# Kernel tuning notes

Hardware: AMD Instinct MI355X
Metric: run time of the kernel (lower is better)

Reference implementation:

```python
import jax, jax.numpy as jnp
import numpy as np

R = 4  # num_relations


def rgcn_conv(x, src, dst, etype, W, root, bias):
    """PyG RGCNConv (aggr='mean', no self-loops):
    out_i = x_i @ root + bias + sum_r mean_{j in N_r(i)} (x_j @ W_r)
    x: [N,D], W: [R,D,H], root: [D,H], bias: [H]
    """
    N = x.shape[0]
    Rr, _, H = W.shape
    x_r = jnp.einsum('nd,rdh->rnh', x, W)          # [R,N,H] relation-transformed feats
    msg = x_r[etype, src]                          # [E,H] per-edge messages
    seg = etype * N + dst                          # combined (relation, dst) segment id
    sums = jax.ops.segment_sum(msg, seg, num_segments=Rr * N)            # [R*N,H]
    cnt = jax.ops.segment_sum(jnp.ones(msg.shape[0], msg.dtype), seg,
                              num_segments=Rr * N)                        # [R*N]
    mean = sums / jnp.maximum(cnt, 1.0)[:, None]
    agg = mean.reshape(Rr, N, H).sum(0)            # sum over relations
    return agg + x @ root + bias


def setup_inputs() -> dict:
    key = jax.random.key(0)
    ks = jax.random.split(key, 12)
    N, E, D, H, ED = 20000, 320000, 256, 256, 64
    s = lambda fan: 1.0 / np.sqrt(fan)
    return {
        'x': jax.random.normal(ks[0], (N, D), jnp.float32),
        'edge_index': jax.random.randint(ks[1], (2, E), 0, N),
        'edge_type': jax.random.randint(ks[2], (E,), 0, R),
        'edge_attr': jax.random.normal(ks[3], (E, ED), jnp.float32),
        'W0': jax.random.normal(ks[4], (R, D, H), jnp.float32) * s(D),
        'root0': jax.random.normal(ks[5], (D, H), jnp.float32) * s(D),
        'b0': jnp.zeros((H,), jnp.float32),
        'W1': jax.random.normal(ks[6], (R, H, H), jnp.float32) * s(H),
        'root1': jax.random.normal(ks[7], (H, H), jnp.float32) * s(H),
        'b1': jnp.zeros((H,), jnp.float32),
        'lin_w': jax.random.normal(ks[8], (H, 2), jnp.float32) * s(H),
        'lin_b': jnp.zeros((2,), jnp.float32),
    }


def reference(x, edge_index, edge_type, edge_attr, W0, root0, b0, W1, root1, b1, lin_w, lin_b):
    src, dst = edge_index[0], edge_index[1]
    h = jax.nn.relu(rgcn_conv(x, src, dst, edge_type, W0, root0, b0))
    h = rgcn_conv(h, src, dst, edge_type, W1, root1, b1)
    g = h.sum(axis=0, keepdims=True)   # global_add_pool, single graph -> [1,H]
    # dropout inactive in eval mode
    return g @ lin_w + lin_b           # [1,2]
```

## Files before the change

### kernel.cpp

```cpp
#include <hip/hip_runtime.h>
#include <hip/hip_bf16.h>

#define RREL 4
#define DIM 256
#define KDIM 1280
#define KMEAN 1024
#define BCAP 32
#define WROWS 64

__device__ __forceinline__ float bf2f(unsigned short u) {
    union { unsigned int i; float f; } z; z.i = ((unsigned int)u) << 16; return z.f;
}
__device__ __forceinline__ unsigned short f2bf(float f) {
    __hip_bfloat16 h = __float2bfloat16(f);
    return *(unsigned short*)&h;
}

typedef __attribute__((ext_vector_type(8))) short bf16x8;
typedef __attribute__((ext_vector_type(8))) unsigned short u16x8;
typedef __attribute__((ext_vector_type(4))) float f32x4;
typedef __attribute__((ext_vector_type(4))) float fx4;


__global__ __launch_bounds__(256)
void prep(const int* __restrict__ etype, const int* __restrict__ src,
          const int* __restrict__ dst,
          int* __restrict__ counts, int* __restrict__ bucket, int N, int E,
          const float* __restrict__ x, __hip_bfloat16* __restrict__ xb, int n4,
          const float* __restrict__ W0, const float* __restrict__ root0,
          __hip_bfloat16* __restrict__ WT,
          int eb, int cb) {
    int b = blockIdx.x;
    if (b < eb) {
        int e = b * 256 + threadIdx.x;
        if (e < E) {
            int seg = etype[e] * N + dst[e];
            int p = atomicAdd(&counts[seg], 1);
            if (p < BCAP) bucket[(size_t)seg * BCAP + p] = src[e];
        }
    } else if (b < eb + cb) {
        int i = (b - eb) * 256 + threadIdx.x;
        if (i < n4) {
            fx4 v = *((const fx4*)x + i);
            ushort4 u = make_ushort4(f2bf(v.x), f2bf(v.y), f2bf(v.z), f2bf(v.w));
            ((ushort4*)xb)[i] = u;
        }
    } else {
        __shared__ float tile[32][33];
        int q = b - eb - cb;
        int nblk = q / 40;
        int kblk = q - nblk * 40;
        int k0 = kblk * 32, n0 = nblk * 32;
        int tx = threadIdx.x & 31, ty = threadIdx.x >> 5;
        const float* srcp;
        int kbase;
        if (k0 < RREL * DIM) { srcp = W0; kbase = k0; } else { srcp = root0; kbase = k0 - RREL * DIM; }
#pragma unroll
        for (int j = 0; j < 4; j++) {
            int k = kbase + ty + j * 8;
            tile[ty + j * 8][tx] = srcp[(size_t)k * DIM + n0 + tx];
        }
        __syncthreads();
#pragma unroll
        for (int j = 0; j < 4; j++) {
            int n = n0 + ty + j * 8;
            WT[(size_t)n * KDIM + k0 + tx] = __float2bfloat16(tile[tx][ty + j * 8]);
        }
    }
}


__global__ __launch_bounds__(256)
void aggregate(const __hip_bfloat16* __restrict__ feat, const int* __restrict__ counts,
               const int* __restrict__ bucket, __hip_bfloat16* __restrict__ Y, int N,
               const int* __restrict__ etype, const int* __restrict__ srcv,
               const int* __restrict__ dstv, float* __restrict__ wsr, int E, int ab) {
    if ((int)blockIdx.x >= ab) {
        int e = (blockIdx.x - ab) * 256 + threadIdx.x;
        if (e < E) {
            int r = etype[e];
            int seg = r * N + dstv[e];
            float sc = 1.f / (float)counts[seg];
            atomicAdd(&wsr[(size_t)srcv[e] * RREL + r], sc);
        }
        return;
    }
    int r = threadIdx.x >> 6, lane = threadIdx.x & 63;
    int h = lane >> 5, li = lane & 31;
    int i = blockIdx.x * 2 + h;
    if (i >= N) return;
    int seg = r * N + i;
    int cnt = min(counts[seg], BCAP);
    const unsigned short* fu = (const unsigned short*)feat;
    const int* bk = bucket + (size_t)seg * BCAP;
    float a[8] = {};
    for (int k = 0; k < cnt; k += 4) {
        int4 q = *(const int4*)(bk + k);
        float m1 = (k + 1 < cnt) ? 1.f : 0.f;
        float m2 = (k + 2 < cnt) ? 1.f : 0.f;
        float m3 = (k + 3 < cnt) ? 1.f : 0.f;
        int i0 = q.x;
        int i1 = m1 ? q.y : q.x;
        int i2 = m2 ? q.z : q.x;
        int i3 = m3 ? q.w : q.x;
        u16x8 v0 = *(const u16x8*)(fu + (size_t)i0 * DIM + li * 8);
        u16x8 v1 = *(const u16x8*)(fu + (size_t)i1 * DIM + li * 8);
        u16x8 v2 = *(const u16x8*)(fu + (size_t)i2 * DIM + li * 8);
        u16x8 v3 = *(const u16x8*)(fu + (size_t)i3 * DIM + li * 8);
#pragma unroll
        for (int j = 0; j < 8; j++)
            a[j] += bf2f(v0[j]) + m1 * bf2f(v1[j]) + m2 * bf2f(v2[j]) + m3 * bf2f(v3[j]);
    }
    float inv = (cnt > 0) ? 1.f / (float)cnt : 0.f;
    u16x8 u;
#pragma unroll
    for (int j = 0; j < 8; j++) u[j] = f2bf(a[j] * inv);
    __builtin_nontemporal_store(u,
        (u16x8*)((unsigned short*)Y + (size_t)i * KMEAN + r * DIM + li * 8));
}


#define BMg 64
#define BKg 64

__global__ __launch_bounds__(256)
void gemm_mfma(const __hip_bfloat16* __restrict__ A,
               const __hip_bfloat16* __restrict__ Aself,
               const __hip_bfloat16* __restrict__ Bt,
               const float* __restrict__ bias,
               unsigned short* __restrict__ Cbf,
               int Nrows) {
    __shared__ short As[2][BMg * BKg];
    __shared__ short Bs[2][DIM * BKg];
    int t = threadIdx.x;
    int lane = t & 63;
    int w = t >> 6;
    size_t row0 = (size_t)blockIdx.x * BMg;

    const unsigned short* Ag = (const unsigned short*)A;
    const unsigned short* Sg = (const unsigned short*)Aself;
    const unsigned short* Bg = (const unsigned short*)Bt;

    float bb[4];
#pragma unroll
    for (int ni = 0; ni < 4; ni++) bb[ni] = bias[w * 64 + ni * 16 + (lane & 15)];

    f32x4 acc[4][4] = {};

    auto issue_tile = [&](int k0, short* as, short* bs) {
        const unsigned short* Abase;
        int kk, stride;
        if (k0 < KMEAN) { Abase = Ag; kk = k0; stride = KMEAN; }
        else            { Abase = Sg; kk = k0 - KMEAN; stride = DIM; }
#pragma unroll
        for (int h = 0; h < 2; h++) {
            int c = t + h * 256;
            int r = c >> 3, pl = c & 7, pg = pl ^ (r & 7);
            const unsigned short* ga = Abase + (row0 + r) * stride + kk + pg * 8;
            __builtin_amdgcn_global_load_lds(
                (const __attribute__((address_space(1))) void*)ga,
                (__attribute__((address_space(3))) void*)((char*)as + c * 16),
                16, 0, 0);
        }
#pragma unroll
        for (int h = 0; h < 8; h++) {
            int c = t + h * 256;
            int r = c >> 3, pl = c & 7, pg = pl ^ (r & 7);
            const unsigned short* gb = Bg + (size_t)r * KDIM + k0 + pg * 8;
            __builtin_amdgcn_global_load_lds(
                (const __attribute__((address_space(1))) void*)gb,
                (__attribute__((address_space(3))) void*)((char*)bs + c * 16),
                16, 0, 0);
        }
    };

    issue_tile(0, As[0], Bs[0]);
    int cur = 0;
    for (int k0 = 0; k0 < KDIM; k0 += BKg) {
        __syncthreads();
        if (k0 + BKg < KDIM) issue_tile(k0 + BKg, As[cur ^ 1], Bs[cur ^ 1]);
        const short* as = As[cur];
        const short* bs = Bs[cur];
#pragma unroll
        for (int ks = 0; ks < 2; ks++) {
            int p = ks * 4 + (lane >> 4);
            bf16x8 af[4], bfr[4];
#pragma unroll
            for (int mi = 0; mi < 4; mi++) {
                int m = mi * 16 + (lane & 15);
                af[mi] = *(const bf16x8*)&as[m * 64 + (p ^ (m & 7)) * 8];
            }
#pragma unroll
            for (int ni = 0; ni < 4; ni++) {
                int n = w * 64 + ni * 16 + (lane & 15);
                bfr[ni] = *(const bf16x8*)&bs[n * 64 + (p ^ (n & 7)) * 8];
            }
#pragma unroll
            for (int mi = 0; mi < 4; mi++)
#pragma unroll
                for (int ni = 0; ni < 4; ni++)
                    acc[mi][ni] = __builtin_amdgcn_mfma_f32_16x16x32_bf16(af[mi], bfr[ni], acc[mi][ni], 0, 0, 0);
        }
        cur ^= 1;
    }

#pragma unroll
    for (int mi = 0; mi < 4; mi++) {
#pragma unroll
        for (int j = 0; j < 4; j++) {
            size_t row = row0 + mi * 16 + (lane >> 4) * 4 + j;
            if (row < (size_t)Nrows) {
#pragma unroll
                for (int ni = 0; ni < 4; ni++) {
                    size_t col = w * 64 + ni * 16 + (lane & 15);
                    float v = fmaxf(acc[mi][ni][j] + bb[ni], 0.f);
                    Cbf[row * DIM + col] = f2bf(v);
                }
            }
        }
    }
}


__global__ __launch_bounds__(256)
void wcolsum(const unsigned short* __restrict__ h1, const float* __restrict__ wsr,
             int N, float* __restrict__ sv) {
    int t = threadIdx.x;
    int i0 = blockIdx.x * WROWS;
    int iend = min(i0 + WROWS, N);
    float a0 = 0.f, a1 = 0.f, a2 = 0.f, a3 = 0.f, as = 0.f;
#pragma unroll 4
    for (int i = i0; i < iend; i++) {
        float v = bf2f(h1[(size_t)i * DIM + t]);
        fx4 wv = *(const fx4*)(wsr + (size_t)i * RREL);
        as += v;
        a0 += wv.x * v; a1 += wv.y * v; a2 += wv.z * v; a3 += wv.w * v;
    }
    atomicAdd(&sv[0 * DIM + t], a0);
    atomicAdd(&sv[1 * DIM + t], a1);
    atomicAdd(&sv[2 * DIM + t], a2);
    atomicAdd(&sv[3 * DIM + t], a3);
    atomicAdd(&sv[4 * DIM + t], as);
}


__global__ __launch_bounds__(256)
void gemv(const float* __restrict__ sv, const float* __restrict__ W1,
          const float* __restrict__ root1, const float* __restrict__ b1,
          int N, float* __restrict__ g) {
    int t = threadIdx.x;
    int kk0 = blockIdx.x * 32;
    float acc = 0.f;
    for (int kk = kk0; kk < kk0 + 32; kk++) {
        int r = kk >> 8;
        int k = kk & 255;
        const float* row = (r < RREL) ? (W1 + ((size_t)r * DIM + k) * DIM)
                                      : (root1 + (size_t)k * DIM);
        acc += sv[kk] * row[t];
    }
    if (blockIdx.x == 0) acc += (float)N * b1[t];
    atomicAdd(&g[t], acc);
}


__global__ void final_lin(const float* __restrict__ g, const float* __restrict__ lw,
                          const float* __restrict__ lb, float* __restrict__ out) {
    __shared__ float s0[256], s1[256];
    int t = threadIdx.x;
    float gv = g[t];
    s0[t] = gv * lw[t * 2 + 0];
    s1[t] = gv * lw[t * 2 + 1];
    __syncthreads();
    for (int off = 128; off > 0; off >>= 1) {
        if (t < off) { s0[t] += s0[t + off]; s1[t] += s1[t + off]; }
        __syncthreads();
    }
    if (t == 0) { out[0] = s0[0] + lb[0]; out[1] = s1[0] + lb[1]; }
}


static inline char* align_up(char* p, size_t a) {
    return (char*)(((uintptr_t)p + (a - 1)) & ~(uintptr_t)(a - 1));
}

extern "C" void kernel_launch(void* const* d_in, const int* in_sizes, int n_in,
                              void* d_out, int out_size, void* d_ws, size_t ws_size,
                              hipStream_t stream) {
    const float* x     = (const float*)d_in[0];
    const int*   eidx  = (const int*)d_in[1];
    const int*   etype = (const int*)d_in[2];
    const float* W0    = (const float*)d_in[4];
    const float* root0 = (const float*)d_in[5];
    const float* b0    = (const float*)d_in[6];
    const float* W1    = (const float*)d_in[7];
    const float* root1 = (const float*)d_in[8];
    const float* b1    = (const float*)d_in[9];
    const float* lin_w = (const float*)d_in[10];
    const float* lin_b = (const float*)d_in[11];
    float* out = (float*)d_out;

    const int N = in_sizes[0] / DIM;
    const int E = in_sizes[2];
    const int RN = RREL * N;
    const int* src = eidx;
    const int* dst = eidx + E;

    const int gx = (N + BMg - 1) / BMg;
    const int Mpad = gx * BMg;

    char* w = (char*)d_ws;
    int*   counts = (int*)w;   w += (size_t)RN * 4;
    float* wsr    = (float*)w; w += (size_t)N * RREL * 4;
    float* sv     = (float*)w; w += (size_t)5 * DIM * 4;
    float* g      = (float*)w; w += 256 * 4;
    size_t zero_bytes = (size_t)RN * 4 + (size_t)N * RREL * 4 + 5 * DIM * 4 + 256 * 4;
    int* bucket = (int*)w; w += (size_t)RN * BCAP * 4;
    w = align_up(w, 16);
    __hip_bfloat16* WT = (__hip_bfloat16*)w; w += (size_t)DIM * KDIM * 2;
    w = align_up(w, 16);
    __hip_bfloat16* Y  = (__hip_bfloat16*)w; w += (size_t)Mpad * KMEAN * 2;
    __hip_bfloat16* xb = (__hip_bfloat16*)w; w += (size_t)Mpad * DIM * 2;
    __hip_bfloat16* h1 = (__hip_bfloat16*)w; w += (size_t)Mpad * DIM * 2;

    hipMemsetAsync(counts, 0, zero_bytes, stream);

    int eb = (E + 255) / 256;
    int n4 = N * DIM / 4;
    int cb = (n4 + 255) / 256;
    int wb = (KDIM / 32) * (DIM / 32);

    prep<<<eb + cb + wb, 256, 0, stream>>>(etype, src, dst, counts, bucket, N, E,
                                           x, xb, n4, W0, root0, WT, eb, cb);

    int ab = (N + 1) / 2;
    aggregate<<<ab + eb, 256, 0, stream>>>(xb, counts, bucket, Y, N,
                                           etype, src, dst, wsr, E, ab);
    gemm_mfma<<<gx, 256, 0, stream>>>(Y, xb, WT, b0, (unsigned short*)h1, N);
    wcolsum<<<(N + WROWS - 1) / WROWS, 256, 0, stream>>>((const unsigned short*)h1, wsr, N, sv);
    gemv<<<KDIM / 32, 256, 0, stream>>>(sv, W1, root1, b1, N, g);

    final_lin<<<1, 256, 0, stream>>>(g, lin_w, lin_b, out);
}
```

Measured before the change: 256.7 us.

## Fuse weighted column-sum into GEMM epilogue and merge gemv with final linear

The GEMM epilogue now computes per-column sums of the ReLU output, plus sums weighted by the relation weights, directly from the accumulators. It reduces them across lanes with shuffles and atomically adds them into sv. This removes the h1 buffer write/read and the separate wcolsum launch. The gemv kernel also absorbs final_lin through a last-block-done counter, saving a launch, at the cost of extra atomics and a fence.

```diff
diff --git a/kernel.cpp b/kernel.cpp
--- a/kernel.cpp
+++ b/kernel.cpp
@@ -6,7 +6,6 @@
 #define KDIM 1280
 #define KMEAN 1024
 #define BCAP 32
-#define WROWS 64
 
 __device__ __forceinline__ float bf2f(unsigned short u) {
     union { unsigned int i; float f; } z; z.i = ((unsigned int)u) << 16; return z.f;
@@ -128,7 +127,8 @@
                const __hip_bfloat16* __restrict__ Aself,
                const __hip_bfloat16* __restrict__ Bt,
                const float* __restrict__ bias,
-               unsigned short* __restrict__ Cbf,
+               const float* __restrict__ wsr,
+               float* __restrict__ sv,
                int Nrows) {
     __shared__ short As[2][BMg * BKg];
     __shared__ short Bs[2][DIM * BKg];
@@ -204,50 +204,51 @@
         cur ^= 1;
     }
 
+    float a[4][5];
+#pragma unroll
+    for (int ni = 0; ni < 4; ni++)
+#pragma unroll
+        for (int s = 0; s < 5; s++) a[ni][s] = 0.f;
+
 #pragma unroll
     for (int mi = 0; mi < 4; mi++) {
 #pragma unroll
         for (int j = 0; j < 4; j++) {
             size_t row = row0 + mi * 16 + (lane >> 4) * 4 + j;
             if (row < (size_t)Nrows) {
+                fx4 wv = *(const fx4*)(wsr + row * RREL);
 #pragma unroll
                 for (int ni = 0; ni < 4; ni++) {
-                    size_t col = w * 64 + ni * 16 + (lane & 15);
                     float v = fmaxf(acc[mi][ni][j] + bb[ni], 0.f);
-                    Cbf[row * DIM + col] = f2bf(v);
+                    a[ni][4] += v;
+                    a[ni][0] += wv.x * v;
+                    a[ni][1] += wv.y * v;
+                    a[ni][2] += wv.z * v;
+                    a[ni][3] += wv.w * v;
                 }
             }
         }
     }
+#pragma unroll
+    for (int ni = 0; ni < 4; ni++) {
+        int col = w * 64 + ni * 16 + (lane & 15);
+#pragma unroll
+        for (int s = 0; s < 5; s++) {
+            float v = a[ni][s];
+            v += __shfl_xor(v, 16, 64);
+            v += __shfl_xor(v, 32, 64);
+            if ((lane >> 4) == 0) atomicAdd(&sv[s * DIM + col], v);
+        }
+    }
 }
 
 
 __global__ __launch_bounds__(256)
-void wcolsum(const unsigned short* __restrict__ h1, const float* __restrict__ wsr,
-             int N, float* __restrict__ sv) {
-    int t = threadIdx.x;
-    int i0 = blockIdx.x * WROWS;
-    int iend = min(i0 + WROWS, N);
-    float a0 = 0.f, a1 = 0.f, a2 = 0.f, a3 = 0.f, as = 0.f;
-#pragma unroll 4
-    for (int i = i0; i < iend; i++) {
-        float v = bf2f(h1[(size_t)i * DIM + t]);
-        fx4 wv = *(const fx4*)(wsr + (size_t)i * RREL);
-        as += v;
-        a0 += wv.x * v; a1 += wv.y * v; a2 += wv.z * v; a3 += wv.w * v;
-    }
-    atomicAdd(&sv[0 * DIM + t], a0);
-    atomicAdd(&sv[1 * DIM + t], a1);
-    atomicAdd(&sv[2 * DIM + t], a2);
-    atomicAdd(&sv[3 * DIM + t], a3);
-    atomicAdd(&sv[4 * DIM + t], as);
-}
-
-
-__global__ __launch_bounds__(256)
-void gemv(const float* __restrict__ sv, const float* __restrict__ W1,
-          const float* __restrict__ root1, const float* __restrict__ b1,
-          int N, float* __restrict__ g) {
+void gemv_final(const float* __restrict__ sv, const float* __restrict__ W1,
+                const float* __restrict__ root1, const float* __restrict__ b1,
+                int N, float* __restrict__ g, int* __restrict__ done,
+                const float* __restrict__ lw, const float* __restrict__ lb,
+                float* __restrict__ out, int nblk) {
     int t = threadIdx.x;
     int kk0 = blockIdx.x * 32;
     float acc = 0.f;
@@ -260,14 +261,13 @@
     }
     if (blockIdx.x == 0) acc += (float)N * b1[t];
     atomicAdd(&g[t], acc);
-}
-
-
-__global__ void final_lin(const float* __restrict__ g, const float* __restrict__ lw,
-                          const float* __restrict__ lb, float* __restrict__ out) {
+    __threadfence();
+    __shared__ int amLast;
+    if (t == 0) amLast = (atomicAdd(done, 1) == nblk - 1);
+    __syncthreads();
+    if (!amLast) return;
+    float gv = atomicAdd(&g[t], 0.f);
     __shared__ float s0[256], s1[256];
-    int t = threadIdx.x;
-    float gv = g[t];
     s0[t] = gv * lw[t * 2 + 0];
     s1[t] = gv * lw[t * 2 + 1];
     __syncthreads();
@@ -313,14 +313,14 @@
     float* wsr    = (float*)w; w += (size_t)N * RREL * 4;
     float* sv     = (float*)w; w += (size_t)5 * DIM * 4;
     float* g      = (float*)w; w += 256 * 4;
-    size_t zero_bytes = (size_t)RN * 4 + (size_t)N * RREL * 4 + 5 * DIM * 4 + 256 * 4;
+    int*   done   = (int*)w;   w += 256;
+    size_t zero_bytes = (size_t)RN * 4 + (size_t)N * RREL * 4 + 5 * DIM * 4 + 256 * 4 + 256;
     int* bucket = (int*)w; w += (size_t)RN * BCAP * 4;
     w = align_up(w, 16);
     __hip_bfloat16* WT = (__hip_bfloat16*)w; w += (size_t)DIM * KDIM * 2;
     w = align_up(w, 16);
     __hip_bfloat16* Y  = (__hip_bfloat16*)w; w += (size_t)Mpad * KMEAN * 2;
     __hip_bfloat16* xb = (__hip_bfloat16*)w; w += (size_t)Mpad * DIM * 2;
-    __hip_bfloat16* h1 = (__hip_bfloat16*)w; w += (size_t)Mpad * DIM * 2;
 
     hipMemsetAsync(counts, 0, zero_bytes, stream);
 
@@ -335,9 +335,8 @@
     int ab = (N + 1) / 2;
     aggregate<<<ab + eb, 256, 0, stream>>>(xb, counts, bucket, Y, N,
                                            etype, src, dst, wsr, E, ab);
-    gemm_mfma<<<gx, 256, 0, stream>>>(Y, xb, WT, b0, (unsigned short*)h1, N);
-    wcolsum<<<(N + WROWS - 1) / WROWS, 256, 0, stream>>>((const unsigned short*)h1, wsr, N, sv);
-    gemv<<<KDIM / 32, 256, 0, stream>>>(sv, W1, root1, b1, N, g);
-
-    final_lin<<<1, 256, 0, stream>>>(g, lin_w, lin_b, out);
-}
+    gemm_mfma<<<gx, 256, 0, stream>>>(Y, xb, WT, b0, wsr, sv, N);
+    int gvb = KDIM / 32;
+    gemv_final<<<gvb, 256, 0, stream>>>(sv, W1, root1, b1, N, g, done,
+                                        lin_w, lin_b, out, gvb);
+}
```

Measured after the change: 248.4 us. -3.2%, faster.
